# Kernel tuning notes

Hardware: AMD Instinct MI355X
Metric: run time of the kernel (lower is better)

Reference implementation:

```python
import jax, jax.numpy as jnp
import numpy as np
import math

HEADS = 8


def sinusoidal_pe_2d(C, H, W, dtype=jnp.float32):
    """Standard fixed 2D sinusoidal PE. Returns (C, H*W).
    First C/2 channels encode row (H) position, last C/2 encode column (W)."""
    half = C // 2
    div = jnp.exp(-math.log(10000.0) * jnp.arange(0, half, 2, dtype=dtype) / half)  # (half/2,)
    pos_h = jnp.arange(H, dtype=dtype)[:, None] * div[None, :]  # (H, half/2)
    pos_w = jnp.arange(W, dtype=dtype)[:, None] * div[None, :]  # (W, half/2)
    # interleave sin/cos along channel dim -> (H, half), (W, half)
    pe_h = jnp.stack([jnp.sin(pos_h), jnp.cos(pos_h)], axis=-1).reshape(H, half)
    pe_w = jnp.stack([jnp.sin(pos_w), jnp.cos(pos_w)], axis=-1).reshape(W, half)
    pe = jnp.concatenate([
        jnp.broadcast_to(pe_h.T[:, :, None], (half, H, W)),
        jnp.broadcast_to(pe_w.T[:, None, :], (half, H, W)),
    ], axis=0)  # (C, H, W)
    return pe.reshape(C, H * W)


def setup_inputs() -> dict:
    key = jax.random.key(0)
    k1, k2, k3, k4 = jax.random.split(key, 4)
    B, c_in, H, W = 16, 256, 64, 64
    c_out = 512
    s = 1.0 / math.sqrt(c_in)
    return {
        "x": jax.random.normal(k1, (B, c_in, H, W), dtype=jnp.float32),
        "Wq": jax.random.normal(k2, (c_out, c_in), dtype=jnp.float32) * s,
        "Wk": jax.random.normal(k3, (c_out, c_in), dtype=jnp.float32) * s,
        "Wv": jax.random.normal(k4, (c_out, c_in), dtype=jnp.float32) * s,
    }


def reference(x, Wq, Wk, Wv):
    B, C, H, W = x.shape
    M = H * W
    c_out = Wq.shape[0]
    heads = HEADS
    dh = c_out // heads
    scale = 1.0 / math.sqrt(dh)

    xf = x.reshape(B, C, M)
    # 1x1 convs (no bias) == channel matmuls
    q = jnp.einsum('oc,bcm->bom', Wq, xf).reshape(B, heads, dh, M)
    k = jnp.einsum('oc,bcm->bom', Wk, xf).reshape(B, heads, dh, M)
    v = jnp.einsum('oc,bcm->bom', Wv, xf).reshape(B, heads, dh, M)

    r = sinusoidal_pe_2d(c_out, H, W, dtype=x.dtype).reshape(1, heads, dh, M)
    q = (jax.nn.elu(q + r) + 1.0) * scale  # feature map phi(q)
    k = (jax.nn.elu(k) + 1.0) * scale      # feature map phi(k)

    KV = jnp.einsum('bhcm,bhdm->bhcd', k, v)          # (B,h,dh,dh)
    out = jnp.einsum('bhcd,bhcm->bhdm', KV, q)        # (B,h,dh,M)
    k_sum = k.sum(axis=-1)                            # (B,h,dh)
    denom = jnp.einsum('bhcm,bhc->bhm', q, k_sum)
    denom = jnp.maximum(denom, 1e-6)[:, :, None, :]   # (B,h,1,M)
    out = out / denom
    return out.reshape(B, c_out, H, W)
```

## Files before the change

### kernel.cpp

```cpp
#include <hip/hip_runtime.h>

#define NB   16
#define CIN  256
#define MM   4096
#define COUT 512
#define NH   8
#define DH   64
#define SCALE 0.125f

typedef __attribute__((ext_vector_type(8))) short bf16x8;
typedef __attribute__((ext_vector_type(4))) float f32x4;

#define PEH_OFF   0u
#define PEW_OFF   65536u
#define WQ_OFF    131072u
#define WKV_OFF   393216u
#define KVP_OFF   917504u
#define KSP_OFF   9306112u
#define AEXT_OFF  9437184u
#define XT_OFF    27787264u
#define WS_NEED   61341696ull

__device__ __forceinline__ unsigned short f2bf(float f) {
    unsigned int u = __float_as_uint(f);
    u = (u + 0x7FFFu + ((u >> 16) & 1u)) >> 16;
    return (unsigned short)u;
}
__device__ __forceinline__ float phi_elu(float x) {
    return (x >= 0.f ? x + 1.f : __expf(x)) * SCALE;
}
__device__ __forceinline__ void gload_lds16(const void* g, void* l) {
    __builtin_amdgcn_global_load_lds(
        (const __attribute__((address_space(1))) unsigned int*)g,
        (__attribute__((address_space(3))) unsigned int*)l, 16, 0, 0);
}

__global__ void k_prep(const float* __restrict__ Wq, const float* __restrict__ Wk,
                       const float* __restrict__ Wv, char* __restrict__ ws) {
    int idx = blockIdx.x * 256 + threadIdx.x;
    if (idx < 32768) {
        int which = idx >> 14;
        int r = idx & 16383;
        int c = r >> 6, pos = r & 63;
        float div = __expf(-logf(10000.f) * (float)(c >> 1) * (1.f / 128.f));
        float t = (float)pos * div;
        float v = (c & 1) ? cosf(t) : sinf(t);
        ((float*)(ws + (which ? PEW_OFF : PEH_OFF)))[r] = v;
        return;
    }
    idx -= 32768;
    if (idx < COUT * CIN) {
        ((unsigned short*)(ws + WQ_OFF))[idx] = f2bf(Wq[idx]);
        return;
    }
    idx -= COUT * CIN;
    if (idx < NH * 128 * CIN) {
        int h = idx >> 15;
        int r = idx & 32767;
        int row = r >> 8, c = r & 255;
        float v = (row < 64) ? Wk[(h * 64 + row) * CIN + c]
                             : Wv[(h * 64 + row - 64) * CIN + c];
        ((unsigned short*)(ws + WKV_OFF))[idx] = f2bf(v);
    }
}


__global__ __launch_bounds__(256) void k_xpose(const float* __restrict__ x, char* __restrict__ ws) {
    __shared__ unsigned short tile[64 * 64];
    int t = threadIdx.x;
    int gx = blockIdx.x;
    int ct = gx & 3, mt = (gx >> 2) & 63, b = gx >> 8;
    int m0 = mt * 64, c0 = ct * 64;
    const float* xb = x + ((size_t)b * CIN + c0) * MM + m0;
    int m4 = (t & 15) * 4;
    int cp0 = (t >> 4) * 2;
#pragma unroll
    for (int p = 0; p < 2; ++p) {
        int cp = cp0 + p * 32;
        float4 v0 = *(const float4*)(xb + (size_t)cp * MM + m4);
        float4 v1 = *(const float4*)(xb + (size_t)(cp + 1) * MM + m4);
        float a0[4] = {v0.x, v0.y, v0.z, v0.w};
        float a1[4] = {v1.x, v1.y, v1.z, v1.w};
#pragma unroll
        for (int i = 0; i < 4; ++i) {
            int m = m4 + i;
            unsigned pk = (unsigned)f2bf(a0[i]) | ((unsigned)f2bf(a1[i]) << 16);
            unsigned off = (unsigned)(m * 128) + (((unsigned)(cp * 2)) ^ ((unsigned)(m & 7) << 4));
            *(unsigned*)((char*)tile + off) = pk;
        }
    }
    __syncthreads();
    unsigned short* xt = (unsigned short*)(ws + XT_OFF) + ((size_t)b * MM + m0) * CIN + c0;
#pragma unroll
    for (int p = 0; p < 2; ++p) {
        int id = t + p * 256;
        int m = id >> 3, u = id & 7;
        unsigned off = (unsigned)(m * 128) + (((unsigned)(u ^ (m & 7))) << 4);
        *(bf16x8*)(xt + (size_t)m * CIN + u * 8) = *(const bf16x8*)((const char*)tile + off);
    }
}

__device__ __forceinline__ void stage_half(const unsigned short* __restrict__ tile_base, int h,
                                           unsigned short* __restrict__ buf, int l, int w) {
#pragma unroll
    for (int i = 0; i < 4; ++i) {
        int r0 = w * 16 + i * 4;
        int m = r0 + (l >> 4);
        unsigned u = (unsigned)(l & 15) ^ (unsigned)(m & 7);
        const char* g = (const char*)tile_base + m * 512 + h * 256 + u * 16;
        gload_lds16(g, (char*)buf + r0 * 256);
    }
}
__device__ __forceinline__ bf16x8 ldsBh(const unsigned short* buf, int n, int k) {
    unsigned off = (unsigned)(n * 256) + (((((unsigned)k) >> 3) ^ ((unsigned)n & 7)) << 4);
    return *(const bf16x8*)((const char*)buf + off);
}

__global__ __launch_bounds__(256) void k_kv4(const char* __restrict__ ws) {
    __shared__ unsigned short bufA[64 * 128];
    __shared__ unsigned short bufB[64 * 128];
    __shared__ unsigned short kt[64 * 72];
    __shared__ unsigned short vt[64 * 72];
    int t = threadIdx.x, l = t & 63, w = t >> 6;
    int blk = blockIdx.x;
    int s = blk & 3, bh = blk >> 2;
    int b = bh >> 3, h = bh & 7;
    const unsigned short* xtb = (const unsigned short*)(ws + XT_OFF) + (size_t)b * MM * CIN;
    const unsigned short* wkv = (const unsigned short*)(ws + WKV_OFF) + (size_t)h * 128 * CIN;
    bf16x8 wreg[2][8];
#pragma unroll
    for (int rf = 0; rf < 2; ++rf)
#pragma unroll
        for (int kk = 0; kk < 8; ++kk)
            wreg[rf][kk] = *(const bf16x8*)(wkv + (size_t)(w * 32 + rf * 16 + (l & 15)) * CIN + kk * 32 + (l >> 4) * 8);

    f32x4 kvacc[4] = {};
    float ksum[2][4] = {};

    const unsigned short* tile0 = xtb + (size_t)(s * 1024) * CIN;
    stage_half(tile0, 0, bufA, l, w);
    __syncthreads();

    for (int ms = 0; ms < 16; ++ms) {
        const unsigned short* tilep = xtb + (size_t)(s * 1024 + ms * 64) * CIN;
        stage_half(tilep, 1, bufB, l, w);

        f32x4 acc[2][4] = {};
#pragma unroll
        for (int kk = 0; kk < 4; ++kk) {
            bf16x8 bfr[4];
#pragma unroll
            for (int cf = 0; cf < 4; ++cf)
                bfr[cf] = ldsBh(bufA, cf * 16 + (l & 15), kk * 32 + (l >> 4) * 8);
#pragma unroll
            for (int rf = 0; rf < 2; ++rf)
#pragma unroll
                for (int cf = 0; cf < 4; ++cf)
                    acc[rf][cf] = __builtin_amdgcn_mfma_f32_16x16x32_bf16(wreg[rf][kk], bfr[cf], acc[rf][cf], 0, 0, 0);
        }
        __syncthreads();

        if (ms < 15)
            stage_half(tilep + 64 * CIN, 0, bufA, l, w);
#pragma unroll
        for (int kk = 0; kk < 4; ++kk) {
            bf16x8 bfr[4];
#pragma unroll
            for (int cf = 0; cf < 4; ++cf)
                bfr[cf] = ldsBh(bufB, cf * 16 + (l & 15), kk * 32 + (l >> 4) * 8);
#pragma unroll
            for (int rf = 0; rf < 2; ++rf)
#pragma unroll
                for (int cf = 0; cf < 4; ++cf)
                    acc[rf][cf] = __builtin_amdgcn_mfma_f32_16x16x32_bf16(wreg[rf][4 + kk], bfr[cf], acc[rf][cf], 0, 0, 0);
        }
        if (w < 2) {
#pragma unroll
            for (int rf = 0; rf < 2; ++rf)
#pragma unroll
                for (int cf = 0; cf < 4; ++cf)
#pragma unroll
                    for (int r = 0; r < 4; ++r) {
                        float p = phi_elu(acc[rf][cf][r]);
                        ksum[rf][r] += p;
                        kt[(w * 32 + rf * 16 + ((l >> 4) << 2) + r) * 72 + cf * 16 + (l & 15)] = f2bf(p);
                    }
        } else {
#pragma unroll
            for (int rf = 0; rf < 2; ++rf)
#pragma unroll
                for (int cf = 0; cf < 4; ++cf)
#pragma unroll
                    for (int r = 0; r < 4; ++r)
                        vt[((w - 2) * 32 + rf * 16 + ((l >> 4) << 2) + r) * 72 + cf * 16 + (l & 15)] = f2bf(acc[rf][cf][r]);
        }
        __syncthreads();
#pragma unroll
        for (int kk = 0; kk < 2; ++kk) {
            bf16x8 a = *(const bf16x8*)(kt + (w * 16 + (l & 15)) * 72 + kk * 32 + (l >> 4) * 8);
#pragma unroll
            for (int cf = 0; cf < 4; ++cf) {
                bf16x8 bb = *(const bf16x8*)(vt + (cf * 16 + (l & 15)) * 72 + kk * 32 + (l >> 4) * 8);
                kvacc[cf] = __builtin_amdgcn_mfma_f32_16x16x32_bf16(a, bb, kvacc[cf], 0, 0, 0);
            }
        }
    }

    float* kvp = (float*)(ws + KVP_OFF) + ((size_t)(bh * 4 + s)) * 4096;
#pragma unroll
    for (int cf = 0; cf < 4; ++cf)
#pragma unroll
        for (int r = 0; r < 4; ++r) {
            int c = w * 16 + ((l >> 4) << 2) + r;
            kvp[c * 64 + cf * 16 + (l & 15)] = kvacc[cf][r];
        }
    if (w < 2) {
        float* ksp = (float*)(ws + KSP_OFF) + (bh * 4 + s) * 64;
#pragma unroll
        for (int rf = 0; rf < 2; ++rf)
#pragma unroll
            for (int r = 0; r < 4; ++r) {
                float v = ksum[rf][r];
                v += __shfl_xor(v, 1); v += __shfl_xor(v, 2);
                v += __shfl_xor(v, 4); v += __shfl_xor(v, 8);
                if ((l & 15) == 0)
                    ksp[w * 32 + rf * 16 + ((l >> 4) << 2) + r] = v;
            }
    }
}

__global__ void k_reduce(char* __restrict__ ws) {
    int bh = blockIdx.x;
    const float* kvp = (const float*)(ws + KVP_OFF) + (size_t)bh * 4 * 4096;
    const float* ksp = (const float*)(ws + KSP_OFF) + bh * 4 * 64;
    unsigned short* a = (unsigned short*)(ws + AEXT_OFF) + (size_t)bh * 80 * 64;
    for (int i = threadIdx.x; i < 80 * 64; i += 256) {
        int d = i >> 6, c = i & 63;
        float v = 0.f;
        if (d < 64) {
#pragma unroll
            for (int s = 0; s < 4; ++s) v += kvp[s * 4096 + c * 64 + d];
        } else if (d == 64) {
#pragma unroll
            for (int s = 0; s < 4; ++s) v += ksp[s * 64 + c];
        }
        a[i] = f2bf(v);
    }
}

__global__ __launch_bounds__(256) void k_out4(const char* __restrict__ ws, float* __restrict__ out) {
    __shared__ unsigned short bufA[64 * 128];
    __shared__ unsigned short bufB[64 * 128];
    __shared__ unsigned short qt[64 * 64];
    __shared__ unsigned short aext[80 * 72];
    int t = threadIdx.x, l = t & 63, w = t >> 6;
    int blk = blockIdx.x;
    int chunk = blk & 3, bh = blk >> 2;
    int b = bh >> 3, h = bh & 7;

    const unsigned short* asrc = (const unsigned short*)(ws + AEXT_OFF) + (size_t)bh * 80 * 64;
    for (int i = t; i < 80 * 8; i += 256) {
        int row = i >> 3, ch = i & 7;
        *(bf16x8*)(aext + row * 72 + ch * 8) = *(const bf16x8*)(asrc + row * 64 + ch * 8);
    }
    const unsigned short* xtb = (const unsigned short*)(ws + XT_OFF) + (size_t)b * MM * CIN;
    const unsigned short* wq = (const unsigned short*)(ws + WQ_OFF);
    bf16x8 wreg[2][8];
#pragma unroll
    for (int rf = 0; rf < 2; ++rf)
#pragma unroll
        for (int kk = 0; kk < 8; ++kk)
            wreg[rf][kk] = *(const bf16x8*)(wq + (size_t)(h * 64 + (w >> 1) * 32 + rf * 16 + (l & 15)) * CIN + kk * 32 + (l >> 4) * 8);

    const float* pe = (h < 4) ? (const float*)(ws + PEH_OFF) : (const float*)(ws + PEW_OFF);
    int obase = h * 64 - (h < 4 ? 0 : 256);
    float* outbh = out + ((size_t)(b * COUT + h * DH)) * MM;

    const unsigned short* tile0 = xtb + (size_t)(chunk * 1024) * CIN;
    stage_half(tile0, 0, bufA, l, w);
    __syncthreads();

    for (int ms = 0; ms < 16; ++ms) {
        int m0 = chunk * 1024 + ms * 64;
        const unsigned short* tilep = xtb + (size_t)m0 * CIN;
        stage_half(tilep, 1, bufB, l, w);

        f32x4 acc[2][2] = {};
#pragma unroll
        for (int kk = 0; kk < 4; ++kk) {
            bf16x8 bfr[2];
#pragma unroll
            for (int mf = 0; mf < 2; ++mf)
                bfr[mf] = ldsBh(bufA, (w & 1) * 32 + mf * 16 + (l & 15), kk * 32 + (l >> 4) * 8);
#pragma unroll
            for (int rf = 0; rf < 2; ++rf)
#pragma unroll
                for (int mf = 0; mf < 2; ++mf)
                    acc[rf][mf] = __builtin_amdgcn_mfma_f32_16x16x32_bf16(wreg[rf][kk], bfr[mf], acc[rf][mf], 0, 0, 0);
        }
        __syncthreads();

        if (ms < 15)
            stage_half(tilep + 64 * CIN, 0, bufA, l, w);
#pragma unroll
        for (int kk = 0; kk < 4; ++kk) {
            bf16x8 bfr[2];
#pragma unroll
            for (int mf = 0; mf < 2; ++mf)
                bfr[mf] = ldsBh(bufB, (w & 1) * 32 + mf * 16 + (l & 15), kk * 32 + (l >> 4) * 8);
#pragma unroll
            for (int rf = 0; rf < 2; ++rf)
#pragma unroll
                for (int mf = 0; mf < 2; ++mf)
                    acc[rf][mf] = __builtin_amdgcn_mfma_f32_16x16x32_bf16(wreg[rf][4 + kk], bfr[mf], acc[rf][mf], 0, 0, 0);
        }
        int im = m0 >> 6;
#pragma unroll
        for (int rf = 0; rf < 2; ++rf) {
#pragma unroll
            for (int mf = 0; mf < 2; ++mf) {
                int mloc = (w & 1) * 32 + mf * 16 + (l & 15);
#pragma unroll
                for (int r = 0; r < 4; ++r) {
                    int c = (w >> 1) * 32 + rf * 16 + ((l >> 4) << 2) + r;
                    int o = obase + c;
                    float pev = (h < 4) ? pe[o * 64 + im] : pe[o * 64 + mloc];
                    float v = phi_elu(acc[rf][mf][r] + pev);
                    unsigned off = (unsigned)(mloc * 128) + (((unsigned)(c * 2)) ^ ((unsigned)(mloc & 7) << 4));
                    *(unsigned short*)((char*)qt + off) = f2bf(v);
                }
            }
        }
        __syncthreads();

        f32x4 acc2[5] = {};
#pragma unroll
        for (int kk = 0; kk < 2; ++kk) {
            int m = w * 16 + (l & 15);
            unsigned koff = (unsigned)(kk * 64 + (l >> 4) * 16);
            unsigned off = (unsigned)(m * 128) + (koff ^ ((unsigned)(m & 7) << 4));
            bf16x8 bb = *(const bf16x8*)((const char*)qt + off);
#pragma unroll
            for (int rf = 0; rf < 5; ++rf) {
                bf16x8 a = *(const bf16x8*)(aext + (rf * 16 + (l & 15)) * 72 + kk * 32 + (l >> 4) * 8);
                acc2[rf] = __builtin_amdgcn_mfma_f32_16x16x32_bf16(a, bb, acc2[rf], 0, 0, 0);
            }
        }
        float den = __shfl(acc2[4][0], l & 15);
        float inv = 1.f / fmaxf(den, 1e-6f);
        int mcol = m0 + w * 16 + (l & 15);
#pragma unroll
        for (int rf = 0; rf < 4; ++rf)
#pragma unroll
            for (int r = 0; r < 4; ++r)
                outbh[(size_t)(rf * 16 + ((l >> 4) << 2) + r) * MM + mcol] = acc2[rf][r] * inv;
    }
}


template<int NTHR>
__device__ __forceinline__ void stage_xT(const float* __restrict__ xb, int m0,
                                         unsigned short* __restrict__ lds, int t) {
    int mg = t & 15;
    for (int c = (t >> 4); c < CIN; c += NTHR / 16) {
        const float* src = xb + c * MM + m0 + mg;
#pragma unroll
        for (int j = 0; j < 4; ++j) {
            int m = mg + 16 * j;
            unsigned off = (unsigned)(m * 512) + (((unsigned)(c * 2)) ^ ((unsigned)(m & 7) << 4));
            *(unsigned short*)((char*)lds + off) = f2bf(src[16 * j]);
        }
    }
}
__device__ __forceinline__ bf16x8 ldsB(const unsigned short* lds, int n, int k) {
    unsigned off = (unsigned)(n * 512) + (((unsigned)(k * 2)) ^ ((unsigned)(n & 7) << 4));
    return *(const bf16x8*)((const char*)lds + off);
}

__global__ __launch_bounds__(512) void k_qgemm(const float* __restrict__ x,
                                               const char* __restrict__ ws,
                                               float* __restrict__ out) {
    __shared__ unsigned short xT[64 * 256];
    int t = threadIdx.x, l = t & 63, w = t >> 6;
    int gx = blockIdx.x;
    int rt = gx & 1;
    int ct = gx >> 1;
    int b = ct >> 6;
    int m0 = (ct & 63) * 64;
    const float* xb = x + (size_t)b * CIN * MM;

    const unsigned short* wq = (const unsigned short*)(ws + WQ_OFF);
    int r0 = rt * 256 + w * 32;
    bf16x8 wreg[2][8];
#pragma unroll
    for (int rf = 0; rf < 2; ++rf)
#pragma unroll
        for (int kk = 0; kk < 8; ++kk)
            wreg[rf][kk] = *(const bf16x8*)(wq + (size_t)(r0 + rf * 16 + (l & 15)) * CIN + kk * 32 + (l >> 4) * 8);

    stage_xT<512>(xb, m0, xT, t);
    __syncthreads();

    f32x4 acc[2][4] = {};
#pragma unroll
    for (int kk = 0; kk < 8; ++kk) {
        bf16x8 bfr[4];
#pragma unroll
        for (int cf = 0; cf < 4; ++cf)
            bfr[cf] = ldsB(xT, cf * 16 + (l & 15), kk * 32 + (l >> 4) * 8);
#pragma unroll
        for (int rf = 0; rf < 2; ++rf)
#pragma unroll
            for (int cf = 0; cf < 4; ++cf)
                acc[rf][cf] = __builtin_amdgcn_mfma_f32_16x16x32_bf16(wreg[rf][kk], bfr[cf], acc[rf][cf], 0, 0, 0);
    }

    const float* peh = (const float*)(ws + PEH_OFF);
    const float* pew = (const float*)(ws + PEW_OFF);
    int im = m0 >> 6;
#pragma unroll
    for (int rf = 0; rf < 2; ++rf) {
#pragma unroll
        for (int cf = 0; cf < 4; ++cf) {
            int mloc = cf * 16 + (l & 15);
#pragma unroll
            for (int r = 0; r < 4; ++r) {
                int o = r0 + rf * 16 + ((l >> 4) << 2) + r;
                float pe = (rt == 0) ? peh[o * 64 + im] : pew[(o - 256) * 64 + mloc];
                float v = phi_elu(acc[rf][cf][r] + pe);
                out[((size_t)(b * COUT + o)) * MM + m0 + mloc] = v;
            }
        }
    }
}

__global__ __launch_bounds__(256) void k_kv(const float* __restrict__ x,
                                            char* __restrict__ ws) {
    __shared__ unsigned short xT[64 * 256];
    __shared__ unsigned short kt[64 * 72];
    __shared__ unsigned short vt[64 * 72];
    int t = threadIdx.x, l = t & 63, w = t >> 6;
    int blk = blockIdx.x;
    int s = blk & 3;
    int bh = blk >> 2;
    int b = bh >> 3, h = bh & 7;
    const float* xb = x + (size_t)b * CIN * MM;

    const unsigned short* wkv = (const unsigned short*)(ws + WKV_OFF) + (size_t)h * 128 * CIN;
    bf16x8 wreg[2][8];
#pragma unroll
    for (int rf = 0; rf < 2; ++rf)
#pragma unroll
        for (int kk = 0; kk < 8; ++kk)
            wreg[rf][kk] = *(const bf16x8*)(wkv + (size_t)(w * 32 + rf * 16 + (l & 15)) * CIN + kk * 32 + (l >> 4) * 8);

    f32x4 kvacc[4] = {};
    float ksum[2][4] = {};

    for (int ms = 0; ms < 16; ++ms) {
        int m0 = s * 1024 + ms * 64;
        if (ms) __syncthreads();
        stage_xT<256>(xb, m0, xT, t);
        __syncthreads();

        f32x4 acc[2][4] = {};
#pragma unroll
        for (int kk = 0; kk < 8; ++kk) {
            bf16x8 bfr[4];
#pragma unroll
            for (int cf = 0; cf < 4; ++cf)
                bfr[cf] = ldsB(xT, cf * 16 + (l & 15), kk * 32 + (l >> 4) * 8);
#pragma unroll
            for (int rf = 0; rf < 2; ++rf)
#pragma unroll
                for (int cf = 0; cf < 4; ++cf)
                    acc[rf][cf] = __builtin_amdgcn_mfma_f32_16x16x32_bf16(wreg[rf][kk], bfr[cf], acc[rf][cf], 0, 0, 0);
        }

        if (w < 2) {
#pragma unroll
            for (int rf = 0; rf < 2; ++rf)
#pragma unroll
                for (int cf = 0; cf < 4; ++cf)
#pragma unroll
                    for (int r = 0; r < 4; ++r) {
                        float p = phi_elu(acc[rf][cf][r]);
                        ksum[rf][r] += p;
                        kt[(w * 32 + rf * 16 + ((l >> 4) << 2) + r) * 72 + cf * 16 + (l & 15)] = f2bf(p);
                    }
        } else {
#pragma unroll
            for (int rf = 0; rf < 2; ++rf)
#pragma unroll
                for (int cf = 0; cf < 4; ++cf)
#pragma unroll
                    for (int r = 0; r < 4; ++r)
                        vt[((w - 2) * 32 + rf * 16 + ((l >> 4) << 2) + r) * 72 + cf * 16 + (l & 15)] = f2bf(acc[rf][cf][r]);
        }
        __syncthreads();

#pragma unroll
        for (int kk = 0; kk < 2; ++kk) {
            bf16x8 a = *(const bf16x8*)(kt + (w * 16 + (l & 15)) * 72 + kk * 32 + (l >> 4) * 8);
#pragma unroll
            for (int cf = 0; cf < 4; ++cf) {
                bf16x8 bb = *(const bf16x8*)(vt + (cf * 16 + (l & 15)) * 72 + kk * 32 + (l >> 4) * 8);
                kvacc[cf] = __builtin_amdgcn_mfma_f32_16x16x32_bf16(a, bb, kvacc[cf], 0, 0, 0);
            }
        }
    }

    float* kvp = (float*)(ws + KVP_OFF) + ((size_t)(bh * 4 + s)) * 64 * 64;
#pragma unroll
    for (int cf = 0; cf < 4; ++cf)
#pragma unroll
        for (int r = 0; r < 4; ++r) {
            int c = w * 16 + ((l >> 4) << 2) + r;
            kvp[c * 64 + cf * 16 + (l & 15)] = kvacc[cf][r];
        }
    if (w < 2) {
        float* ksp = (float*)(ws + KSP_OFF) + (bh * 4 + s) * 64;
#pragma unroll
        for (int rf = 0; rf < 2; ++rf)
#pragma unroll
            for (int r = 0; r < 4; ++r) {
                float v = ksum[rf][r];
                v += __shfl_xor(v, 1); v += __shfl_xor(v, 2);
                v += __shfl_xor(v, 4); v += __shfl_xor(v, 8);
                if ((l & 15) == 0)
                    ksp[w * 32 + rf * 16 + ((l >> 4) << 2) + r] = v;
            }
    }
}

__global__ __launch_bounds__(256) void k_out(const char* __restrict__ ws,
                                             float* __restrict__ out) {
    __shared__ unsigned short aext[80 * 72];
    __shared__ unsigned short qt[64 * 72];
    int t = threadIdx.x, l = t & 63, w = t >> 6;
    int blk = blockIdx.x;
    int chunk = blk & 7, bh = blk >> 3;
    int b = bh >> 3, h = bh & 7;

    const unsigned short* asrc = (const unsigned short*)(ws + AEXT_OFF) + (size_t)bh * 80 * 64;
    for (int i = t; i < 80 * 8; i += 256) {
        int row = i >> 3, ch = i & 7;
        *(bf16x8*)(aext + row * 72 + ch * 8) = *(const bf16x8*)(asrc + row * 64 + ch * 8);
    }
    float* outbh = out + ((size_t)(b * COUT + h * DH)) * MM;

    for (int ms = 0; ms < 8; ++ms) {
        int m0 = chunk * 512 + ms * 64;
        __syncthreads();
        {
            int mg = t & 15;
            for (int c = t >> 4; c < 64; c += 16) {
                const float* src = outbh + (size_t)c * MM + m0 + mg;
#pragma unroll
                for (int j = 0; j < 4; ++j)
                    qt[(mg + 16 * j) * 72 + c] = f2bf(src[16 * j]);
            }
        }
        __syncthreads();
        f32x4 acc[5] = {};
#pragma unroll
        for (int kk = 0; kk < 2; ++kk) {
            bf16x8 bb = *(const bf16x8*)(qt + (w * 16 + (l & 15)) * 72 + kk * 32 + (l >> 4) * 8);
#pragma unroll
            for (int rf = 0; rf < 5; ++rf) {
                bf16x8 a = *(const bf16x8*)(aext + (rf * 16 + (l & 15)) * 72 + kk * 32 + (l >> 4) * 8);
                acc[rf] = __builtin_amdgcn_mfma_f32_16x16x32_bf16(a, bb, acc[rf], 0, 0, 0);
            }
        }
        float den = __shfl(acc[4][0], l & 15);
        float inv = 1.f / fmaxf(den, 1e-6f);
        int mcol = m0 + w * 16 + (l & 15);
#pragma unroll
        for (int rf = 0; rf < 4; ++rf)
#pragma unroll
            for (int r = 0; r < 4; ++r)
                outbh[(size_t)(rf * 16 + ((l >> 4) << 2) + r) * MM + mcol] = acc[rf][r] * inv;
    }
}

extern "C" void kernel_launch(void* const* d_in, const int* in_sizes, int n_in,
                              void* d_out, int out_size, void* d_ws, size_t ws_size,
                              hipStream_t stream) {
    const float* x  = (const float*)d_in[0];
    const float* Wq = (const float*)d_in[1];
    const float* Wk = (const float*)d_in[2];
    const float* Wv = (const float*)d_in[3];
    float* out = (float*)d_out;
    char* ws = (char*)d_ws;

    hipLaunchKernelGGL(k_prep, dim3(1664), dim3(256), 0, stream, Wq, Wk, Wv, ws);
    if (ws_size >= WS_NEED) {
        hipLaunchKernelGGL(k_xpose,  dim3(4096), dim3(256), 0, stream, x, ws);
        hipLaunchKernelGGL(k_kv4,    dim3(512),  dim3(256), 0, stream, ws);
        hipLaunchKernelGGL(k_reduce, dim3(128),  dim3(256), 0, stream, ws);
        hipLaunchKernelGGL(k_out4,   dim3(512),  dim3(256), 0, stream, ws, out);
    } else {
        hipLaunchKernelGGL(k_qgemm,  dim3(2048), dim3(512), 0, stream, x, ws, out);
        hipLaunchKernelGGL(k_kv,     dim3(512),  dim3(256), 0, stream, x, ws);
        hipLaunchKernelGGL(k_reduce, dim3(128),  dim3(256), 0, stream, ws);
        hipLaunchKernelGGL(k_out,    dim3(1024), dim3(256), 0, stream, ws, out);
    }
}
```

Measured before the change: 136.7 us.

## Share staged x tiles across multiple heads in KV and output kernels

The KV kernel now uses 512-thread blocks that cover two heads (K and V) per staged x tile over a 512-position slice, with 8 partial splits reduced by a new reduce kernel. The output kernel handles four heads per block so each staged x tile feeds four heads' Q projection, adding a swizzled LDS copy of the KV/ksum matrices and an LDS denominator exchange. The aim is to cut repeated global/L2 reads of the transposed bf16 x per head. In exchange it uses more LDS and registers per block, has more partial sums to reduce, and runs a smaller grid for the output kernel.

```diff
diff --git a/kernel.cpp b/kernel.cpp
--- a/kernel.cpp
+++ b/kernel.cpp
@@ -18,6 +18,8 @@
 #define KVP_OFF   917504u
 #define KSP_OFF   9306112u
 #define AEXT_OFF  9437184u
+#define KVP2_OFF  10747904u
+#define KSP2_OFF  27525120u
 #define XT_OFF    27787264u
 #define WS_NEED   61341696ull
 
@@ -100,11 +102,12 @@
     }
 }
 
+template<int NW>
 __device__ __forceinline__ void stage_half(const unsigned short* __restrict__ tile_base, int h,
                                            unsigned short* __restrict__ buf, int l, int w) {
 #pragma unroll
-    for (int i = 0; i < 4; ++i) {
-        int r0 = w * 16 + i * 4;
+    for (int i = 0; i < 16 / NW; ++i) {
+        int r0 = w * (64 / NW) + i * 4;
         int m = r0 + (l >> 4);
         unsigned u = (unsigned)(l & 15) ^ (unsigned)(m & 7);
         const char* g = (const char*)tile_base + m * 512 + h * 256 + u * 16;
@@ -116,34 +119,41 @@
     return *(const bf16x8*)((const char*)buf + off);
 }
 
-__global__ __launch_bounds__(256) void k_kv4(const char* __restrict__ ws) {
+__global__ __launch_bounds__(512, 2) void k_kv5(const char* __restrict__ ws) {
     __shared__ unsigned short bufA[64 * 128];
     __shared__ unsigned short bufB[64 * 128];
-    __shared__ unsigned short kt[64 * 72];
-    __shared__ unsigned short vt[64 * 72];
+    __shared__ unsigned short kt[128 * 72];
+    __shared__ unsigned short vt[128 * 72];
     int t = threadIdx.x, l = t & 63, w = t >> 6;
     int blk = blockIdx.x;
-    int s = blk & 3, bh = blk >> 2;
-    int b = bh >> 3, h = bh & 7;
+    int s = blk & 7, rest = blk >> 3;
+    int hg = rest & 3, b = rest >> 2;
     const unsigned short* xtb = (const unsigned short*)(ws + XT_OFF) + (size_t)b * MM * CIN;
-    const unsigned short* wkv = (const unsigned short*)(ws + WKV_OFF) + (size_t)h * 128 * CIN;
+
+    int isv = w >> 2;
+    int wk = w & 3;
+    int hl = wk & 1, rh = wk >> 1;
+    int head = hg * 2 + hl;
+    const unsigned short* wkv = (const unsigned short*)(ws + WKV_OFF) + (size_t)head * 128 * CIN;
+    int rowbase = isv * 64 + rh * 32;
     bf16x8 wreg[2][8];
 #pragma unroll
     for (int rf = 0; rf < 2; ++rf)
 #pragma unroll
         for (int kk = 0; kk < 8; ++kk)
-            wreg[rf][kk] = *(const bf16x8*)(wkv + (size_t)(w * 32 + rf * 16 + (l & 15)) * CIN + kk * 32 + (l >> 4) * 8);
-
-    f32x4 kvacc[4] = {};
+            wreg[rf][kk] = *(const bf16x8*)(wkv + (size_t)(rowbase + rf * 16 + (l & 15)) * CIN + kk * 32 + (l >> 4) * 8);
+
+    f32x4 kvacc[2][2] = {};
     float ksum[2][4] = {};
-
-    const unsigned short* tile0 = xtb + (size_t)(s * 1024) * CIN;
-    stage_half(tile0, 0, bufA, l, w);
+    int wh = w & 1, ch = (w >> 1) & 1, dh = w >> 2;
+
+    const unsigned short* tile0 = xtb + (size_t)(s * 512) * CIN;
+    stage_half<8>(tile0, 0, bufA, l, w);
     __syncthreads();
 
-    for (int ms = 0; ms < 16; ++ms) {
-        const unsigned short* tilep = xtb + (size_t)(s * 1024 + ms * 64) * CIN;
-        stage_half(tilep, 1, bufB, l, w);
+    for (int ms = 0; ms < 8; ++ms) {
+        const unsigned short* tilep = xtb + (size_t)(s * 512 + ms * 64) * CIN;
+        stage_half<8>(tilep, 1, bufB, l, w);
 
         f32x4 acc[2][4] = {};
 #pragma unroll
@@ -160,8 +170,8 @@
         }
         __syncthreads();
 
-        if (ms < 15)
-            stage_half(tilep + 64 * CIN, 0, bufA, l, w);
+        if (ms < 7)
+            stage_half<8>(tilep + 64 * CIN, 0, bufA, l, w);
 #pragma unroll
         for (int kk = 0; kk < 4; ++kk) {
             bf16x8 bfr[4];
@@ -174,7 +184,8 @@
                 for (int cf = 0; cf < 4; ++cf)
                     acc[rf][cf] = __builtin_amdgcn_mfma_f32_16x16x32_bf16(wreg[rf][4 + kk], bfr[cf], acc[rf][cf], 0, 0, 0);
         }
-        if (w < 2) {
+        int ktrow0 = hl * 64 + rh * 32;
+        if (!isv) {
 #pragma unroll
             for (int rf = 0; rf < 2; ++rf)
 #pragma unroll
@@ -183,7 +194,7 @@
                     for (int r = 0; r < 4; ++r) {
                         float p = phi_elu(acc[rf][cf][r]);
                         ksum[rf][r] += p;
-                        kt[(w * 32 + rf * 16 + ((l >> 4) << 2) + r) * 72 + cf * 16 + (l & 15)] = f2bf(p);
+                        kt[(ktrow0 + rf * 16 + ((l >> 4) << 2) + r) * 72 + cf * 16 + (l & 15)] = f2bf(p);
                     }
         } else {
 #pragma unroll
@@ -192,30 +203,40 @@
                 for (int cf = 0; cf < 4; ++cf)
 #pragma unroll
                     for (int r = 0; r < 4; ++r)
-                        vt[((w - 2) * 32 + rf * 16 + ((l >> 4) << 2) + r) * 72 + cf * 16 + (l & 15)] = f2bf(acc[rf][cf][r]);
+                        vt[(ktrow0 + rf * 16 + ((l >> 4) << 2) + r) * 72 + cf * 16 + (l & 15)] = f2bf(acc[rf][cf][r]);
         }
         __syncthreads();
 #pragma unroll
         for (int kk = 0; kk < 2; ++kk) {
-            bf16x8 a = *(const bf16x8*)(kt + (w * 16 + (l & 15)) * 72 + kk * 32 + (l >> 4) * 8);
-#pragma unroll
-            for (int cf = 0; cf < 4; ++cf) {
-                bf16x8 bb = *(const bf16x8*)(vt + (cf * 16 + (l & 15)) * 72 + kk * 32 + (l >> 4) * 8);
-                kvacc[cf] = __builtin_amdgcn_mfma_f32_16x16x32_bf16(a, bb, kvacc[cf], 0, 0, 0);
-            }
-        }
-    }
-
-    float* kvp = (float*)(ws + KVP_OFF) + ((size_t)(bh * 4 + s)) * 4096;
-#pragma unroll
-    for (int cf = 0; cf < 4; ++cf)
-#pragma unroll
-        for (int r = 0; r < 4; ++r) {
-            int c = w * 16 + ((l >> 4) << 2) + r;
-            kvp[c * 64 + cf * 16 + (l & 15)] = kvacc[cf][r];
-        }
-    if (w < 2) {
-        float* ksp = (float*)(ws + KSP_OFF) + (bh * 4 + s) * 64;
+            bf16x8 a[2], bb[2];
+#pragma unroll
+            for (int rf = 0; rf < 2; ++rf)
+                a[rf] = *(const bf16x8*)(kt + (wh * 64 + ch * 32 + rf * 16 + (l & 15)) * 72 + kk * 32 + (l >> 4) * 8);
+#pragma unroll
+            for (int cf = 0; cf < 2; ++cf)
+                bb[cf] = *(const bf16x8*)(vt + (wh * 64 + dh * 32 + cf * 16 + (l & 15)) * 72 + kk * 32 + (l >> 4) * 8);
+#pragma unroll
+            for (int rf = 0; rf < 2; ++rf)
+#pragma unroll
+                for (int cf = 0; cf < 2; ++cf)
+                    kvacc[rf][cf] = __builtin_amdgcn_mfma_f32_16x16x32_bf16(a[rf], bb[cf], kvacc[rf][cf], 0, 0, 0);
+        }
+    }
+
+    int bhk = b * 8 + hg * 2 + wh;
+    float* kvp = (float*)(ws + KVP2_OFF) + ((size_t)(bhk * 8 + s)) * 4096;
+#pragma unroll
+    for (int rf = 0; rf < 2; ++rf)
+#pragma unroll
+        for (int cf = 0; cf < 2; ++cf)
+#pragma unroll
+            for (int r = 0; r < 4; ++r) {
+                int c = ch * 32 + rf * 16 + ((l >> 4) << 2) + r;
+                int d = dh * 32 + cf * 16 + (l & 15);
+                kvp[c * 64 + d] = kvacc[rf][cf][r];
+            }
+    if (!isv) {
+        float* ksp = (float*)(ws + KSP2_OFF) + ((size_t)(b * 8 + head) * 8 + s) * 64;
 #pragma unroll
         for (int rf = 0; rf < 2; ++rf)
 #pragma unroll
@@ -224,136 +245,159 @@
                 v += __shfl_xor(v, 1); v += __shfl_xor(v, 2);
                 v += __shfl_xor(v, 4); v += __shfl_xor(v, 8);
                 if ((l & 15) == 0)
-                    ksp[w * 32 + rf * 16 + ((l >> 4) << 2) + r] = v;
-            }
-    }
-}
-
-__global__ void k_reduce(char* __restrict__ ws) {
+                    ksp[rh * 32 + rf * 16 + ((l >> 4) << 2) + r] = v;
+            }
+    }
+}
+
+__global__ void k_reduce2(char* __restrict__ ws) {
     int bh = blockIdx.x;
-    const float* kvp = (const float*)(ws + KVP_OFF) + (size_t)bh * 4 * 4096;
-    const float* ksp = (const float*)(ws + KSP_OFF) + bh * 4 * 64;
+    const float* kvp = (const float*)(ws + KVP2_OFF) + (size_t)bh * 8 * 4096;
+    const float* ksp = (const float*)(ws + KSP2_OFF) + bh * 8 * 64;
     unsigned short* a = (unsigned short*)(ws + AEXT_OFF) + (size_t)bh * 80 * 64;
     for (int i = threadIdx.x; i < 80 * 64; i += 256) {
         int d = i >> 6, c = i & 63;
         float v = 0.f;
         if (d < 64) {
 #pragma unroll
-            for (int s = 0; s < 4; ++s) v += kvp[s * 4096 + c * 64 + d];
+            for (int s = 0; s < 8; ++s) v += kvp[s * 4096 + c * 64 + d];
         } else if (d == 64) {
 #pragma unroll
-            for (int s = 0; s < 4; ++s) v += ksp[s * 64 + c];
+            for (int s = 0; s < 8; ++s) v += ksp[s * 64 + c];
         }
         a[i] = f2bf(v);
     }
 }
 
-__global__ __launch_bounds__(256) void k_out4(const char* __restrict__ ws, float* __restrict__ out) {
+__global__ __launch_bounds__(512, 2) void k_out5(const char* __restrict__ ws, float* __restrict__ out) {
     __shared__ unsigned short bufA[64 * 128];
     __shared__ unsigned short bufB[64 * 128];
-    __shared__ unsigned short qt[64 * 64];
-    __shared__ unsigned short aext[80 * 72];
+    __shared__ unsigned short qt[4 * 64 * 64];
+    __shared__ unsigned short ax[4 * 80 * 64];
+    __shared__ float den[4 * 64];
     int t = threadIdx.x, l = t & 63, w = t >> 6;
     int blk = blockIdx.x;
-    int chunk = blk & 3, bh = blk >> 2;
-    int b = bh >> 3, h = bh & 7;
-
-    const unsigned short* asrc = (const unsigned short*)(ws + AEXT_OFF) + (size_t)bh * 80 * 64;
-    for (int i = t; i < 80 * 8; i += 256) {
-        int row = i >> 3, ch = i & 7;
-        *(bf16x8*)(aext + row * 72 + ch * 8) = *(const bf16x8*)(asrc + row * 64 + ch * 8);
-    }
-    const unsigned short* xtb = (const unsigned short*)(ws + XT_OFF) + (size_t)b * MM * CIN;
+    int chunk = blk & 7, rest = blk >> 3;
+    int hg = rest & 1, b = rest >> 1;
+
+    const unsigned short* asrc = (const unsigned short*)(ws + AEXT_OFF) + (size_t)(b * 8 + hg * 4) * 80 * 64;
+    for (int i = t; i < 4 * 80 * 8; i += 512) {
+        int h = i / 640, rem = i % 640, row = rem >> 3, u = rem & 7;
+        bf16x8 v = *(const bf16x8*)(asrc + ((size_t)h * 80 + row) * 64 + u * 8);
+        unsigned dst = (unsigned)((h * 80 + row) * 128) + ((((unsigned)u) ^ ((unsigned)row & 7)) << 4);
+        *(bf16x8*)((char*)ax + dst) = v;
+    }
+
+    int h = w >> 1, rh = w & 1;
+    int hglob = hg * 4 + h;
     const unsigned short* wq = (const unsigned short*)(ws + WQ_OFF);
     bf16x8 wreg[2][8];
 #pragma unroll
     for (int rf = 0; rf < 2; ++rf)
 #pragma unroll
         for (int kk = 0; kk < 8; ++kk)
-            wreg[rf][kk] = *(const bf16x8*)(wq + (size_t)(h * 64 + (w >> 1) * 32 + rf * 16 + (l & 15)) * CIN + kk * 32 + (l >> 4) * 8);
-
-    const float* pe = (h < 4) ? (const float*)(ws + PEH_OFF) : (const float*)(ws + PEW_OFF);
-    int obase = h * 64 - (h < 4 ? 0 : 256);
-    float* outbh = out + ((size_t)(b * COUT + h * DH)) * MM;
-
-    const unsigned short* tile0 = xtb + (size_t)(chunk * 1024) * CIN;
-    stage_half(tile0, 0, bufA, l, w);
+            wreg[rf][kk] = *(const bf16x8*)(wq + (size_t)(hglob * 64 + rh * 32 + rf * 16 + (l & 15)) * CIN + kk * 32 + (l >> 4) * 8);
+
+    const float* peh = (const float*)(ws + PEH_OFF);
+    const float* pew = (const float*)(ws + PEW_OFF);
+    float* outb = out + ((size_t)(b * COUT + hglob * 64)) * MM;
+    const unsigned short* xtb = (const unsigned short*)(ws + XT_OFF) + (size_t)b * MM * CIN;
+
+    const unsigned short* tile0 = xtb + (size_t)(chunk * 512) * CIN;
+    stage_half<8>(tile0, 0, bufA, l, w);
     __syncthreads();
 
-    for (int ms = 0; ms < 16; ++ms) {
-        int m0 = chunk * 1024 + ms * 64;
+    for (int ms = 0; ms < 8; ++ms) {
+        int m0 = chunk * 512 + ms * 64;
         const unsigned short* tilep = xtb + (size_t)m0 * CIN;
-        stage_half(tilep, 1, bufB, l, w);
-
-        f32x4 acc[2][2] = {};
+        stage_half<8>(tilep, 1, bufB, l, w);
+
+        f32x4 acc[2][4] = {};
 #pragma unroll
         for (int kk = 0; kk < 4; ++kk) {
-            bf16x8 bfr[2];
-#pragma unroll
-            for (int mf = 0; mf < 2; ++mf)
-                bfr[mf] = ldsBh(bufA, (w & 1) * 32 + mf * 16 + (l & 15), kk * 32 + (l >> 4) * 8);
-#pragma unroll
-            for (int rf = 0; rf < 2; ++rf)
-#pragma unroll
-                for (int mf = 0; mf < 2; ++mf)
-                    acc[rf][mf] = __builtin_amdgcn_mfma_f32_16x16x32_bf16(wreg[rf][kk], bfr[mf], acc[rf][mf], 0, 0, 0);
-        }
-        __syncthreads();
-
-        if (ms < 15)
-            stage_half(tilep + 64 * CIN, 0, bufA, l, w);
+            bf16x8 bfr[4];
+#pragma unroll
+            for (int cf = 0; cf < 4; ++cf)
+                bfr[cf] = ldsBh(bufA, cf * 16 + (l & 15), kk * 32 + (l >> 4) * 8);
+#pragma unroll
+            for (int rf = 0; rf < 2; ++rf)
+#pragma unroll
+                for (int cf = 0; cf < 4; ++cf)
+                    acc[rf][cf] = __builtin_amdgcn_mfma_f32_16x16x32_bf16(wreg[rf][kk], bfr[cf], acc[rf][cf], 0, 0, 0);
+        }
+        __syncthreads();
+
+        if (ms < 7)
+            stage_half<8>(tilep + 64 * CIN, 0, bufA, l, w);
 #pragma unroll
         for (int kk = 0; kk < 4; ++kk) {
-            bf16x8 bfr[2];
-#pragma unroll
-            for (int mf = 0; mf < 2; ++mf)
-                bfr[mf] = ldsBh(bufB, (w & 1) * 32 + mf * 16 + (l & 15), kk * 32 + (l >> 4) * 8);
-#pragma unroll
-            for (int rf = 0; rf < 2; ++rf)
-#pragma unroll
-                for (int mf = 0; mf < 2; ++mf)
-                    acc[rf][mf] = __builtin_amdgcn_mfma_f32_16x16x32_bf16(wreg[rf][4 + kk], bfr[mf], acc[rf][mf], 0, 0, 0);
+            bf16x8 bfr[4];
+#pragma unroll
+            for (int cf = 0; cf < 4; ++cf)
+                bfr[cf] = ldsBh(bufB, cf * 16 + (l & 15), kk * 32 + (l >> 4) * 8);
+#pragma unroll
+            for (int rf = 0; rf < 2; ++rf)
+#pragma unroll
+                for (int cf = 0; cf < 4; ++cf)
+                    acc[rf][cf] = __builtin_amdgcn_mfma_f32_16x16x32_bf16(wreg[rf][4 + kk], bfr[cf], acc[rf][cf], 0, 0, 0);
         }
         int im = m0 >> 6;
 #pragma unroll
-        for (int rf = 0; rf < 2; ++rf) {
-#pragma unroll
-            for (int mf = 0; mf < 2; ++mf) {
-                int mloc = (w & 1) * 32 + mf * 16 + (l & 15);
+        for (int rf = 0; rf < 2; ++rf)
+#pragma unroll
+            for (int cf = 0; cf < 4; ++cf) {
+                int mloc = cf * 16 + (l & 15);
 #pragma unroll
                 for (int r = 0; r < 4; ++r) {
-                    int c = (w >> 1) * 32 + rf * 16 + ((l >> 4) << 2) + r;
-                    int o = obase + c;
-                    float pev = (h < 4) ? pe[o * 64 + im] : pe[o * 64 + mloc];
-                    float v = phi_elu(acc[rf][mf][r] + pev);
-                    unsigned off = (unsigned)(mloc * 128) + (((unsigned)(c * 2)) ^ ((unsigned)(mloc & 7) << 4));
+                    int c = rh * 32 + rf * 16 + ((l >> 4) << 2) + r;
+                    int o = hglob * 64 + c;
+                    float pev = (hglob < 4) ? peh[o * 64 + im] : pew[(o - 256) * 64 + mloc];
+                    float v = phi_elu(acc[rf][cf][r] + pev);
+                    unsigned off = (unsigned)((h * 64 + mloc) * 128) + (((unsigned)(c * 2)) ^ (((unsigned)mloc & 7) << 4));
                     *(unsigned short*)((char*)qt + off) = f2bf(v);
                 }
             }
-        }
-        __syncthreads();
-
-        f32x4 acc2[5] = {};
+        __syncthreads();
+
+        f32x4 acc2[3][4] = {};
+        int nrf = rh ? 2 : 3;
 #pragma unroll
         for (int kk = 0; kk < 2; ++kk) {
-            int m = w * 16 + (l & 15);
-            unsigned koff = (unsigned)(kk * 64 + (l >> 4) * 16);
-            unsigned off = (unsigned)(m * 128) + (koff ^ ((unsigned)(m & 7) << 4));
-            bf16x8 bb = *(const bf16x8*)((const char*)qt + off);
-#pragma unroll
-            for (int rf = 0; rf < 5; ++rf) {
-                bf16x8 a = *(const bf16x8*)(aext + (rf * 16 + (l & 15)) * 72 + kk * 32 + (l >> 4) * 8);
-                acc2[rf] = __builtin_amdgcn_mfma_f32_16x16x32_bf16(a, bb, acc2[rf], 0, 0, 0);
-            }
-        }
-        float den = __shfl(acc2[4][0], l & 15);
-        float inv = 1.f / fmaxf(den, 1e-6f);
-        int mcol = m0 + w * 16 + (l & 15);
-#pragma unroll
-        for (int rf = 0; rf < 4; ++rf)
-#pragma unroll
-            for (int r = 0; r < 4; ++r)
-                outbh[(size_t)(rf * 16 + ((l >> 4) << 2) + r) * MM + mcol] = acc2[rf][r] * inv;
+            bf16x8 bb[4];
+#pragma unroll
+            for (int cf = 0; cf < 4; ++cf) {
+                int m = cf * 16 + (l & 15);
+                unsigned off = (unsigned)((h * 64 + m) * 128) + (((unsigned)(kk * 64 + (l >> 4) * 16)) ^ (((unsigned)m & 7) << 4));
+                bb[cf] = *(const bf16x8*)((const char*)qt + off);
+            }
+            for (int rfl = 0; rfl < nrf; ++rfl) {
+                int rfg = rh ? (2 + rfl) : (rfl < 2 ? rfl : 4);
+                int row = rfg * 16 + (l & 15);
+                unsigned aoff = (unsigned)((h * 80 + row) * 128) + ((((unsigned)(kk * 4 + (l >> 4))) ^ ((unsigned)row & 7)) << 4);
+                bf16x8 a = *(const bf16x8*)((const char*)ax + aoff);
+#pragma unroll
+                for (int cf = 0; cf < 4; ++cf)
+                    acc2[rfl][cf] = __builtin_amdgcn_mfma_f32_16x16x32_bf16(a, bb[cf], acc2[rfl][cf], 0, 0, 0);
+            }
+        }
+        if (!rh && (l >> 4) == 0) {
+#pragma unroll
+            for (int cf = 0; cf < 4; ++cf)
+                den[h * 64 + cf * 16 + l] = acc2[2][cf][0];
+        }
+        __syncthreads();
+#pragma unroll
+        for (int rfl = 0; rfl < 2; ++rfl)
+#pragma unroll
+            for (int cf = 0; cf < 4; ++cf) {
+                int m = cf * 16 + (l & 15);
+                float inv = 1.f / fmaxf(den[h * 64 + m], 1e-6f);
+#pragma unroll
+                for (int r = 0; r < 4; ++r) {
+                    int d = rh * 32 + rfl * 16 + ((l >> 4) << 2) + r;
+                    outb[(size_t)d * MM + m0 + m] = acc2[rfl][cf][r] * inv;
+                }
+            }
     }
 }
 
@@ -533,6 +577,25 @@
     }
 }
 
+__global__ void k_reduce(char* __restrict__ ws) {
+    int bh = blockIdx.x;
+    const float* kvp = (const float*)(ws + KVP_OFF) + (size_t)bh * 4 * 4096;
+    const float* ksp = (const float*)(ws + KSP_OFF) + bh * 4 * 64;
+    unsigned short* a = (unsigned short*)(ws + AEXT_OFF) + (size_t)bh * 80 * 64;
+    for (int i = threadIdx.x; i < 80 * 64; i += 256) {
+        int d = i >> 6, c = i & 63;
+        float v = 0.f;
+        if (d < 64) {
+#pragma unroll
+            for (int s = 0; s < 4; ++s) v += kvp[s * 4096 + c * 64 + d];
+        } else if (d == 64) {
+#pragma unroll
+            for (int s = 0; s < 4; ++s) v += ksp[s * 64 + c];
+        }
+        a[i] = f2bf(v);
+    }
+}
+
 __global__ __launch_bounds__(256) void k_out(const char* __restrict__ ws,
                                              float* __restrict__ out) {
     __shared__ unsigned short aext[80 * 72];
@@ -595,10 +658,10 @@
 
     hipLaunchKernelGGL(k_prep, dim3(1664), dim3(256), 0, stream, Wq, Wk, Wv, ws);
     if (ws_size >= WS_NEED) {
-        hipLaunchKernelGGL(k_xpose,  dim3(4096), dim3(256), 0, stream, x, ws);
-        hipLaunchKernelGGL(k_kv4,    dim3(512),  dim3(256), 0, stream, ws);
-        hipLaunchKernelGGL(k_reduce, dim3(128),  dim3(256), 0, stream, ws);
-        hipLaunchKernelGGL(k_out4,   dim3(512),  dim3(256), 0, stream, ws, out);
+        hipLaunchKernelGGL(k_xpose,   dim3(4096), dim3(256), 0, stream, x, ws);
+        hipLaunchKernelGGL(k_kv5,     dim3(512),  dim3(512), 0, stream, ws);
+        hipLaunchKernelGGL(k_reduce2, dim3(128),  dim3(256), 0, stream, ws);
+        hipLaunchKernelGGL(k_out5,    dim3(256),  dim3(512), 0, stream, ws, out);
     } else {
         hipLaunchKernelGGL(k_qgemm,  dim3(2048), dim3(512), 0, stream, x, ws, out);
         hipLaunchKernelGGL(k_kv,     dim3(512),  dim3(256), 0, stream, x, ws);
```

After: 305.3 us (median of 3 runs). 2.23x slower.
